# Optimization experiments

Hardware: AMD Instinct MI355X
Metric: run time of the kernel (lower is better)

## Reference

```python
import jax, jax.numpy as jnp
import numpy as np

B, N, C, H = 128, 8732, 512, 19  # batch, priors, channels, feature map side
IMG = 300.0
FG = 19


def setup_inputs() -> dict:
    key = jax.random.key(0)
    ks = jax.random.split(key, 10)
    loc = jax.random.normal(ks[0], (B, N, 4), jnp.float32) * 0.5
    conf = jax.random.normal(ks[1], (B, N, 2), jnp.float32)
    priors = jax.random.uniform(ks[2], (N, 4), jnp.float32, minval=0.05, maxval=0.95)
    features = jax.random.normal(ks[3], (B, C, H, H), jnp.float32)
    w1 = jax.random.normal(ks[4], (C, 4096), jnp.float32) * 0.01
    b1 = jnp.zeros((4096,), jnp.float32)
    w2 = jax.random.normal(ks[5], (4096, 4096), jnp.float32) * 0.01
    b2 = jnp.zeros((4096,), jnp.float32)
    w3 = jax.random.normal(ks[6], (4096, FG), jnp.float32) * 0.01
    b3 = jnp.zeros((FG,), jnp.float32)
    return {"loc": loc, "conf": conf, "priors": priors, "features": features,
            "w1": w1, "b1": b1, "w2": w2, "b2": b2, "w3": w3, "b3": b3}


def _decode(loc, priors):
    # SSD decode, variances=[0.1, 0.2]; priors are (cx, cy, w, h)
    cxcy = priors[:, :2] + loc[..., :2] * 0.1 * priors[:, 2:]
    wh = priors[:, 2:] * jnp.exp(loc[..., 2:] * 0.2)
    xy1 = cxcy - 0.5 * wh
    return jnp.concatenate([xy1, xy1 + wh], axis=-1)  # [B,N,4] corner form


def _best_prior(loc, conf, priors):
    boxes = _decode(loc, priors)                       # [B,N,4]
    probs = jax.nn.softmax(conf, axis=-1)              # [B,N,2]
    car = jnp.argmax(probs, axis=-1) == 1              # [B,N] argmax class == car
    score = jnp.where(car, probs[..., 1], -jnp.inf)
    best = jnp.argmax(score, axis=-1)                  # [B]
    best_box = jnp.take_along_axis(boxes, best[:, None, None], axis=1)[:, 0]  # [B,4]
    has_car = jnp.any(car, axis=-1)                    # [B]
    geom = (best_box[:, 2] > best_box[:, 0]) & (best_box[:, 3] > best_box[:, 1])
    valid = has_car & geom
    result = jnp.where(has_car[:, None], best_box, 0.0)
    result = jnp.clip(result, 0.0, 1.0)
    return result, valid


def _extract(features, boxes, valid):
    # per-box crop + global max pool -> [B,C], zero for invalid boxes
    ceil_num = features.shape[2]
    step = IMG / ceil_num
    b = jnp.clip(boxes * IMG, 0.0, IMG) / step
    b = jnp.floor(jnp.clip(b, 0.0, ceil_num - 1.0)).astype(jnp.int32)  # [B,4]=x1,y1,x2,y2
    r = jnp.arange(ceil_num)
    mh = (r[None, :] >= b[:, 1:2]) & (r[None, :] <= b[:, 3:4])  # [B,H] rows
    mw = (r[None, :] >= b[:, 0:1]) & (r[None, :] <= b[:, 2:3])  # [B,W] cols
    mask = mh[:, None, :, None] & mw[:, None, None, :]          # [B,1,H,W]
    m = jnp.max(jnp.where(mask, features, -jnp.inf), axis=(2, 3))  # [B,C]
    return jnp.where(valid[:, None], m, 0.0)


def reference(loc, conf, priors, features, w1, b1, w2, b2, w3, b3):
    boxes, valid = _best_prior(loc, conf, priors)
    feat = _extract(features, boxes, valid)             # [B,512]
    h = jax.nn.relu(feat @ w1 + b1)
    h = jax.nn.relu(h @ w2 + b2)
    fg_cls = h @ w3 + b3                                # [B,19]
    return fg_cls, boxes, valid.astype(jnp.int32)
```

## Files before the change

### kernel.cpp

```cpp
#include <hip/hip_runtime.h>
#include <hip/hip_bf16.h>
#include <math.h>

#define BATCH 128
#define NPRI  8732
#define CCH   512
#define HH    19
#define NHID  4096
#define FGC   19

typedef unsigned short ushort_t;
typedef __attribute__((ext_vector_type(8))) short bf16x8;
typedef __attribute__((ext_vector_type(4))) float f32x4;

__device__ __forceinline__ ushort_t f2bf(float f) {
  unsigned u = __float_as_uint(f);
  u += 0x7fff + ((u >> 16) & 1);
  return (ushort_t)(u >> 16);
}


__global__ void k_best_partial(const float* __restrict__ conf,
                               float* __restrict__ cs, int* __restrict__ ci,
                               int* __restrict__ cc) {
  int blk = blockIdx.x;
  int b = blk >> 2, chunk = blk & 3;
  int n0 = chunk * 2183;
  int t = threadIdx.x;
  const float* cb = conf + (size_t)b * NPRI * 2;
  float bestS = -INFINITY; int bestN = 0x7fffffff; int car_any = 0;
  for (int i = n0 + t; i < n0 + 2183; i += 256) {
    float c0 = cb[2 * i], c1 = cb[2 * i + 1];
    float m = fmaxf(c0, c1);
    float e0 = expf(c0 - m), e1 = expf(c1 - m);
    float s = e0 + e1;
    float p0 = e0 / s, p1 = e1 / s;
    bool car = p1 > p0;
    car_any |= (int)car;
    float sc = car ? p1 : -INFINITY;
    if (sc > bestS || (sc == bestS && i < bestN)) { bestS = sc; bestN = i; }
  }
  __shared__ float ls[256]; __shared__ int li[256]; __shared__ int lc[256];
  ls[t] = bestS; li[t] = bestN; lc[t] = car_any;
  __syncthreads();
  for (int off = 128; off > 0; off >>= 1) {
    if (t < off) {
      float s2 = ls[t + off]; int n2 = li[t + off];
      if (s2 > ls[t] || (s2 == ls[t] && n2 < li[t])) { ls[t] = s2; li[t] = n2; }
      lc[t] |= lc[t + off];
    }
    __syncthreads();
  }
  if (t == 0) { cs[blk] = ls[0]; ci[blk] = li[0]; cc[blk] = lc[0]; }
}

__global__ void k_best_final(const float* __restrict__ loc,
                             const float* __restrict__ priors,
                             const float* __restrict__ cs,
                             const int* __restrict__ ci,
                             const int* __restrict__ cc,
                             float* __restrict__ out_boxes,
                             float* __restrict__ out_valid,
                             int4* __restrict__ crop,
                             int* __restrict__ vflag) {
  int b = threadIdx.x;
  if (b >= BATCH) return;
  float bs = -INFINITY; int bn = 0; int hc = 0;
  #pragma unroll
  for (int p = 0; p < 4; p++) {
    float s = cs[b * 4 + p]; int n = ci[b * 4 + p];
    hc |= cc[b * 4 + p];
    if (s > bs) { bs = s; bn = n; }
  }
  const float* lp = loc + ((size_t)b * NPRI + bn) * 4;
  const float* pp = priors + (size_t)bn * 4;
  float l0 = lp[0], l1 = lp[1], l2 = lp[2], l3 = lp[3];
  float pcx = pp[0], pcy = pp[1], pw = pp[2], ph = pp[3];
  float cx = pcx + (l0 * 0.1f) * pw;
  float cy = pcy + (l1 * 0.1f) * ph;
  float w = pw * expf(l2 * 0.2f);
  float h = ph * expf(l3 * 0.2f);
  float x1 = cx - 0.5f * w;
  float y1 = cy - 0.5f * h;
  float x2 = x1 + w, y2 = y1 + h;
  bool geom = (x2 > x1) && (y2 > y1);
  bool valid = hc && geom;
  float r0, r1, r2, r3;
  if (hc) { r0 = x1; r1 = y1; r2 = x2; r3 = y2; }
  else    { r0 = r1 = r2 = r3 = 0.0f; }
  r0 = fminf(fmaxf(r0, 0.0f), 1.0f);
  r1 = fminf(fmaxf(r1, 0.0f), 1.0f);
  r2 = fminf(fmaxf(r2, 0.0f), 1.0f);
  r3 = fminf(fmaxf(r3, 0.0f), 1.0f);
  out_boxes[b * 4 + 0] = r0; out_boxes[b * 4 + 1] = r1;
  out_boxes[b * 4 + 2] = r2; out_boxes[b * 4 + 3] = r3;
  out_valid[b] = valid ? 1.0f : 0.0f;
  const float stepF = (float)(300.0 / 19.0);
  float q0 = fminf(fmaxf(r0 * 300.0f, 0.0f), 300.0f) / stepF;
  float q1 = fminf(fmaxf(r1 * 300.0f, 0.0f), 300.0f) / stepF;
  float q2 = fminf(fmaxf(r2 * 300.0f, 0.0f), 300.0f) / stepF;
  float q3 = fminf(fmaxf(r3 * 300.0f, 0.0f), 300.0f) / stepF;
  int ix1 = (int)floorf(fminf(fmaxf(q0, 0.0f), 18.0f));
  int iy1 = (int)floorf(fminf(fmaxf(q1, 0.0f), 18.0f));
  int ix2 = (int)floorf(fminf(fmaxf(q2, 0.0f), 18.0f));
  int iy2 = (int)floorf(fminf(fmaxf(q3, 0.0f), 18.0f));
  crop[b] = make_int4(ix1, iy1, ix2, iy2);
  vflag[b] = valid ? 1 : 0;
}

__global__ void k_extract(const float* __restrict__ fin,
                          const int4* __restrict__ crop,
                          const int* __restrict__ vflag,
                          ushort_t* __restrict__ feat) {
  int blk = blockIdx.x;
  int b = blk >> 7;
  int tile = blk & 127;
  int wave = threadIdx.x >> 6;
  int lane = threadIdx.x & 63;
  int c = tile * 4 + wave;
  if (!vflag[b]) {
    if (lane == 0) feat[b * CCH + c] = 0;
    return;
  }
  int4 cr = crop[b];
  int wcnt = cr.z - cr.x + 1;
  int cnt = wcnt * (cr.w - cr.y + 1);
  const float* p = fin + (size_t)(b * CCH + c) * (HH * HH);
  float m = -INFINITY;
  for (int i = lane; i < cnt; i += 64) {
    int yy = cr.y + i / wcnt;
    int xx = cr.x + i % wcnt;
    m = fmaxf(m, p[yy * HH + xx]);
  }
  #pragma unroll
  for (int off = 32; off > 0; off >>= 1) m = fmaxf(m, __shfl_xor(m, off));
  if (lane == 0) feat[b * CCH + c] = f2bf(m);
}

template <int KSPL>
__global__ __launch_bounds__(256) void k_mfma(const ushort_t* __restrict__ A,
                                              const float* __restrict__ W,
                                              float* __restrict__ part, int K) {
  const int N = 4096;
  const int BK = 32;
  int nb = blockIdx.x;
  int ks = blockIdx.y;
  int Kper = K / KSPL;
  int k0b = ks * Kper;
  int t = threadIdx.x;
  int lane = t & 63, wave = t >> 6;
  int q = lane >> 4, r = lane & 15;

  __shared__ ushort_t As[128 * 40];
  __shared__ ushort_t Bs[64 * 40];

  int wm = (wave & 1) * 64;
  int wn = (wave >> 1) * 32;
  int n0 = nb * 64;

  f32x4 acc[4][2];
  #pragma unroll
  for (int i = 0; i < 4; i++)
    #pragma unroll
    for (int j = 0; j < 2; j++) {
      acc[i][j].x = 0.f; acc[i][j].y = 0.f; acc[i][j].z = 0.f; acc[i][j].w = 0.f;
    }

  int am = t >> 1, ah = t & 1;
  int bp = t >> 4;
  int bn = t & 15;

  for (int k0 = k0b; k0 < k0b + Kper; k0 += BK) {
    const uint4* asrc = (const uint4*)(A + (size_t)am * K + k0 + ah * 16);
    uint4 a0 = asrc[0];
    uint4 a1 = asrc[1];
    const float* wsrc = W + (size_t)(k0 + 2 * bp) * N + n0 + bn;
    float wr0[4], wr1[4];
    #pragma unroll
    for (int i = 0; i < 4; i++) {
      wr0[i] = wsrc[16 * i];
      wr1[i] = wsrc[N + 16 * i];
    }
    __syncthreads();
    *(uint4*)&As[am * 40 + ah * 16]     = a0;
    *(uint4*)&As[am * 40 + ah * 16 + 8] = a1;
    #pragma unroll
    for (int i = 0; i < 4; i++) {
      unsigned pk = (unsigned)f2bf(wr0[i]) | ((unsigned)f2bf(wr1[i]) << 16);
      *(unsigned*)&Bs[(bn + 16 * i) * 40 + 2 * bp] = pk;
    }
    __syncthreads();
    bf16x8 af[4], bfr[2];
    #pragma unroll
    for (int i = 0; i < 4; i++)
      af[i] = *(const bf16x8*)&As[(wm + 16 * i + r) * 40 + q * 8];
    #pragma unroll
    for (int j = 0; j < 2; j++)
      bfr[j] = *(const bf16x8*)&Bs[(wn + 16 * j + r) * 40 + q * 8];
    #pragma unroll
    for (int i = 0; i < 4; i++)
      #pragma unroll
      for (int j = 0; j < 2; j++)
        acc[i][j] = __builtin_amdgcn_mfma_f32_16x16x32_bf16(af[i], bfr[j],
                                                            acc[i][j], 0, 0, 0);
  }

  float* dst = part + (size_t)ks * (BATCH * N);
  #pragma unroll
  for (int i = 0; i < 4; i++) {
    #pragma unroll
    for (int j = 0; j < 2; j++) {
      int col = n0 + wn + 16 * j + r;
      #pragma unroll
      for (int reg = 0; reg < 4; reg++) {
        int row = wm + 16 * i + q * 4 + reg;
        dst[(size_t)row * N + col] = acc[i][j][reg];
      }
    }
  }
}

template <int KSPL, bool BF16OUT>
__global__ void k_finalize(const float* __restrict__ part,
                           const float* __restrict__ bias,
                           float* __restrict__ outf,
                           ushort_t* __restrict__ outb) {
  int idx = (blockIdx.x * 256 + threadIdx.x) * 4;
  float4 s = *(const float4*)(part + idx);
  #pragma unroll
  for (int p = 1; p < KSPL; p++) {
    float4 v = *(const float4*)(part + (size_t)p * (BATCH * NHID) + idx);
    s.x += v.x; s.y += v.y; s.z += v.z; s.w += v.w;
  }
  float4 bv = *(const float4*)(bias + (idx & (NHID - 1)));
  s.x = fmaxf(s.x + bv.x, 0.0f); s.y = fmaxf(s.y + bv.y, 0.0f);
  s.z = fmaxf(s.z + bv.z, 0.0f); s.w = fmaxf(s.w + bv.w, 0.0f);
  if (BF16OUT) {
    ushort4 o;
    o.x = f2bf(s.x); o.y = f2bf(s.y); o.z = f2bf(s.z); o.w = f2bf(s.w);
    *(ushort4*)(outb + idx) = o;
  } else {
    *(float4*)(outf + idx) = s;
  }
}

__global__ void k_gemm3p(const float* __restrict__ h2,
                         const float* __restrict__ w3,
                         float* __restrict__ part3) {
  int kc = blockIdx.x;
  int t = threadIdx.x;
  __shared__ float wl[32 * FGC];
  for (int i = t; i < 32 * FGC; i += 128) wl[i] = w3[kc * 32 * FGC + i];
  __syncthreads();
  const float* hp = h2 + (size_t)t * NHID + kc * 32;
  float acc[FGC];
  #pragma unroll
  for (int j = 0; j < FGC; j++) acc[j] = 0.0f;
  for (int k = 0; k < 32; k++) {
    float hv = hp[k];
    const float* wp = &wl[k * FGC];
    #pragma unroll
    for (int j = 0; j < FGC; j++) acc[j] += hv * wp[j];
  }
  float* dst = part3 + (size_t)kc * (BATCH * FGC) + t * FGC;
  #pragma unroll
  for (int j = 0; j < FGC; j++) dst[j] = acc[j];
}

__global__ void k_fin3(const float* __restrict__ part3,
                       const float* __restrict__ b3,
                       float* __restrict__ out) {
  int j = blockIdx.x * 256 + threadIdx.x;
  if (j >= BATCH * FGC) return;
  float s = 0.0f;
  for (int p = 0; p < 128; p++) s += part3[(size_t)p * (BATCH * FGC) + j];
  out[j] = s + b3[j % FGC];
}

extern "C" void kernel_launch(void* const* d_in, const int* in_sizes, int n_in,
                              void* d_out, int out_size, void* d_ws, size_t ws_size,
                              hipStream_t stream) {
  const float* loc      = (const float*)d_in[0];
  const float* conf     = (const float*)d_in[1];
  const float* priors   = (const float*)d_in[2];
  const float* features = (const float*)d_in[3];
  const float* w1 = (const float*)d_in[4];
  const float* b1 = (const float*)d_in[5];
  const float* w2 = (const float*)d_in[6];
  const float* b2 = (const float*)d_in[7];
  const float* w3 = (const float*)d_in[8];
  const float* b3 = (const float*)d_in[9];
  float* out = (float*)d_out;

  char* ws = (char*)d_ws;
  float*    part  = (float*)ws;
  float*    part3 = (float*)(ws + (size_t)16 * 1024 * 1024);
  float*    h2    = (float*)(ws + (size_t)18 * 1024 * 1024);
  ushort_t* featb = (ushort_t*)(ws + (size_t)20 * 1024 * 1024);
  ushort_t* h1b   = (ushort_t*)(ws + (size_t)20 * 1024 * 1024 + 256 * 1024);
  float*    cs    = (float*)(ws + (size_t)21 * 1024 * 1024 + 512 * 1024);
  int*      ci    = (int*)(cs + 512);
  int*      cc    = ci + 512;
  int4*     crop  = (int4*)(cc + 512);
  int*      vfl   = (int*)(crop + BATCH);

  k_best_partial<<<512, 256, 0, stream>>>(conf, cs, ci, cc);
  k_best_final<<<1, 128, 0, stream>>>(loc, priors, cs, ci, cc,
                                      out + BATCH * FGC,
                                      out + BATCH * FGC + BATCH * 4, crop, vfl);
  k_extract<<<BATCH * (CCH / 4), 256, 0, stream>>>(features, crop, vfl, featb);
  k_mfma<4><<<dim3(64, 4), 256, 0, stream>>>(featb, w1, part, 512);
  k_finalize<4, true><<<512, 256, 0, stream>>>(part, b1, nullptr, h1b);
  k_mfma<8><<<dim3(64, 8), 256, 0, stream>>>(h1b, w2, part, 4096);
  k_finalize<8, false><<<512, 256, 0, stream>>>(part, b2, h2, nullptr);
  k_gemm3p<<<128, 128, 0, stream>>>(h2, w3, part3);
  k_fin3<<<10, 256, 0, stream>>>(part3, b3, out);
}
```

Baseline: 263.1 us.

## Merge best-prior kernels, vectorize extract, double-buffer MFMA GEMM, atomic final layer

```diff
diff --git a/kernel.cpp b/kernel.cpp
--- a/kernel.cpp
+++ b/kernel.cpp
@@ -1,5 +1,4 @@
 #include <hip/hip_runtime.h>
-#include <hip/hip_bf16.h>
 #include <math.h>
 
 #define BATCH 128
@@ -9,30 +8,31 @@
 #define NHID  4096
 #define FGC   19
 
-typedef unsigned short ushort_t;
+typedef unsigned short u16;
 typedef __attribute__((ext_vector_type(8))) short bf16x8;
 typedef __attribute__((ext_vector_type(4))) float f32x4;
 
-__device__ __forceinline__ ushort_t f2bf(float f) {
+__device__ __forceinline__ u16 f2bf(float f) {
   unsigned u = __float_as_uint(f);
   u += 0x7fff + ((u >> 16) & 1);
-  return (ushort_t)(u >> 16);
-}
-
-
-__global__ void k_best_partial(const float* __restrict__ conf,
-                               float* __restrict__ cs, int* __restrict__ ci,
-                               int* __restrict__ cc) {
-  int blk = blockIdx.x;
-  int b = blk >> 2, chunk = blk & 3;
-  int n0 = chunk * 2183;
+  return (u16)(u >> 16);
+}
+
+__global__ void k_best(const float* __restrict__ loc,
+                       const float* __restrict__ conf,
+                       const float* __restrict__ priors,
+                       const float* __restrict__ b3,
+                       float* __restrict__ out,
+                       int4* __restrict__ crop,
+                       int* __restrict__ vflag) {
+  int b = blockIdx.x;
   int t = threadIdx.x;
   const float* cb = conf + (size_t)b * NPRI * 2;
   float bestS = -INFINITY; int bestN = 0x7fffffff; int car_any = 0;
-  for (int i = n0 + t; i < n0 + 2183; i += 256) {
-    float c0 = cb[2 * i], c1 = cb[2 * i + 1];
-    float m = fmaxf(c0, c1);
-    float e0 = expf(c0 - m), e1 = expf(c1 - m);
+  for (int i = t; i < NPRI; i += 256) {
+    float2 c = *(const float2*)(cb + 2 * i);
+    float m = fmaxf(c.x, c.y);
+    float e0 = expf(c.x - m), e1 = expf(c.y - m);
     float s = e0 + e1;
     float p0 = e0 / s, p1 = e1 / s;
     bool car = p1 > p0;
@@ -51,112 +51,121 @@
     }
     __syncthreads();
   }
-  if (t == 0) { cs[blk] = ls[0]; ci[blk] = li[0]; cc[blk] = lc[0]; }
-}
-
-__global__ void k_best_final(const float* __restrict__ loc,
-                             const float* __restrict__ priors,
-                             const float* __restrict__ cs,
-                             const int* __restrict__ ci,
-                             const int* __restrict__ cc,
-                             float* __restrict__ out_boxes,
-                             float* __restrict__ out_valid,
-                             int4* __restrict__ crop,
-                             int* __restrict__ vflag) {
-  int b = threadIdx.x;
-  if (b >= BATCH) return;
-  float bs = -INFINITY; int bn = 0; int hc = 0;
-  #pragma unroll
-  for (int p = 0; p < 4; p++) {
-    float s = cs[b * 4 + p]; int n = ci[b * 4 + p];
-    hc |= cc[b * 4 + p];
-    if (s > bs) { bs = s; bn = n; }
-  }
-  const float* lp = loc + ((size_t)b * NPRI + bn) * 4;
-  const float* pp = priors + (size_t)bn * 4;
-  float l0 = lp[0], l1 = lp[1], l2 = lp[2], l3 = lp[3];
-  float pcx = pp[0], pcy = pp[1], pw = pp[2], ph = pp[3];
-  float cx = pcx + (l0 * 0.1f) * pw;
-  float cy = pcy + (l1 * 0.1f) * ph;
-  float w = pw * expf(l2 * 0.2f);
-  float h = ph * expf(l3 * 0.2f);
-  float x1 = cx - 0.5f * w;
-  float y1 = cy - 0.5f * h;
-  float x2 = x1 + w, y2 = y1 + h;
-  bool geom = (x2 > x1) && (y2 > y1);
-  bool valid = hc && geom;
-  float r0, r1, r2, r3;
-  if (hc) { r0 = x1; r1 = y1; r2 = x2; r3 = y2; }
-  else    { r0 = r1 = r2 = r3 = 0.0f; }
-  r0 = fminf(fmaxf(r0, 0.0f), 1.0f);
-  r1 = fminf(fmaxf(r1, 0.0f), 1.0f);
-  r2 = fminf(fmaxf(r2, 0.0f), 1.0f);
-  r3 = fminf(fmaxf(r3, 0.0f), 1.0f);
-  out_boxes[b * 4 + 0] = r0; out_boxes[b * 4 + 1] = r1;
-  out_boxes[b * 4 + 2] = r2; out_boxes[b * 4 + 3] = r3;
-  out_valid[b] = valid ? 1.0f : 0.0f;
-  const float stepF = (float)(300.0 / 19.0);
-  float q0 = fminf(fmaxf(r0 * 300.0f, 0.0f), 300.0f) / stepF;
-  float q1 = fminf(fmaxf(r1 * 300.0f, 0.0f), 300.0f) / stepF;
-  float q2 = fminf(fmaxf(r2 * 300.0f, 0.0f), 300.0f) / stepF;
-  float q3 = fminf(fmaxf(r3 * 300.0f, 0.0f), 300.0f) / stepF;
-  int ix1 = (int)floorf(fminf(fmaxf(q0, 0.0f), 18.0f));
-  int iy1 = (int)floorf(fminf(fmaxf(q1, 0.0f), 18.0f));
-  int ix2 = (int)floorf(fminf(fmaxf(q2, 0.0f), 18.0f));
-  int iy2 = (int)floorf(fminf(fmaxf(q3, 0.0f), 18.0f));
-  crop[b] = make_int4(ix1, iy1, ix2, iy2);
-  vflag[b] = valid ? 1 : 0;
+  if (t < FGC) out[b * FGC + t] = b3[t];
+  if (t == 0) {
+    int hc = lc[0];
+    int bn = hc ? li[0] : 0;
+    const float* lp = loc + ((size_t)b * NPRI + bn) * 4;
+    const float* pp = priors + (size_t)bn * 4;
+    float l0 = lp[0], l1 = lp[1], l2 = lp[2], l3 = lp[3];
+    float pcx = pp[0], pcy = pp[1], pw = pp[2], ph = pp[3];
+    float cx = pcx + (l0 * 0.1f) * pw;
+    float cy = pcy + (l1 * 0.1f) * ph;
+    float w = pw * expf(l2 * 0.2f);
+    float h = ph * expf(l3 * 0.2f);
+    float x1 = cx - 0.5f * w;
+    float y1 = cy - 0.5f * h;
+    float x2 = x1 + w, y2 = y1 + h;
+    bool geom = (x2 > x1) && (y2 > y1);
+    bool valid = hc && geom;
+    float r0, r1, r2, r3;
+    if (hc) { r0 = x1; r1 = y1; r2 = x2; r3 = y2; }
+    else    { r0 = r1 = r2 = r3 = 0.0f; }
+    r0 = fminf(fmaxf(r0, 0.0f), 1.0f);
+    r1 = fminf(fmaxf(r1, 0.0f), 1.0f);
+    r2 = fminf(fmaxf(r2, 0.0f), 1.0f);
+    r3 = fminf(fmaxf(r3, 0.0f), 1.0f);
+    float* ob = out + BATCH * FGC;
+    ob[b * 4 + 0] = r0; ob[b * 4 + 1] = r1;
+    ob[b * 4 + 2] = r2; ob[b * 4 + 3] = r3;
+    out[BATCH * FGC + BATCH * 4 + b] = valid ? 1.0f : 0.0f;
+    const float stepF = (float)(300.0 / 19.0);
+    float q0 = fminf(fmaxf(r0 * 300.0f, 0.0f), 300.0f) / stepF;
+    float q1 = fminf(fmaxf(r1 * 300.0f, 0.0f), 300.0f) / stepF;
+    float q2 = fminf(fmaxf(r2 * 300.0f, 0.0f), 300.0f) / stepF;
+    float q3 = fminf(fmaxf(r3 * 300.0f, 0.0f), 300.0f) / stepF;
+    int ix1 = (int)floorf(fminf(fmaxf(q0, 0.0f), 18.0f));
+    int iy1 = (int)floorf(fminf(fmaxf(q1, 0.0f), 18.0f));
+    int ix2 = (int)floorf(fminf(fmaxf(q2, 0.0f), 18.0f));
+    int iy2 = (int)floorf(fminf(fmaxf(q3, 0.0f), 18.0f));
+    crop[b] = make_int4(ix1, iy1, ix2, iy2);
+    vflag[b] = valid ? 1 : 0;
+  }
 }
 
 __global__ void k_extract(const float* __restrict__ fin,
                           const int4* __restrict__ crop,
                           const int* __restrict__ vflag,
-                          ushort_t* __restrict__ feat) {
-  int blk = blockIdx.x;
-  int b = blk >> 7;
-  int tile = blk & 127;
-  int wave = threadIdx.x >> 6;
-  int lane = threadIdx.x & 63;
-  int c = tile * 4 + wave;
+                          u16* __restrict__ feat) {
+  int b = blockIdx.x >> 3;
+  int cg = blockIdx.x & 7;
+  int wave = threadIdx.x >> 6, lane = threadIdx.x & 63;
   if (!vflag[b]) {
-    if (lane == 0) feat[b * CCH + c] = 0;
+    if (lane == 0) {
+      #pragma unroll
+      for (int ci = 0; ci < 16; ci++) feat[b * CCH + cg * 64 + ci * 4 + wave] = 0;
+    }
     return;
   }
   int4 cr = crop[b];
-  int wcnt = cr.z - cr.x + 1;
-  int cnt = wcnt * (cr.w - cr.y + 1);
-  const float* p = fin + (size_t)(b * CCH + c) * (HH * HH);
-  float m = -INFINITY;
-  for (int i = lane; i < cnt; i += 64) {
-    int yy = cr.y + i / wcnt;
-    int xx = cr.x + i % wcnt;
-    m = fmaxf(m, p[yy * HH + xx]);
-  }
-  #pragma unroll
-  for (int off = 32; off > 0; off >>= 1) m = fmaxf(m, __shfl_xor(m, off));
-  if (lane == 0) feat[b * CCH + c] = f2bf(m);
+  int base = cr.y * HH;
+  int L = (cr.w - cr.y + 1) * HH;
+  int a0 = base & ~3;
+  int offs = base - a0;
+  int total = offs + L;
+  int nf4 = total >> 2, rem = total & 3;
+  int x1 = cr.x, x2 = cr.z;
+  #pragma unroll 4
+  for (int ci = 0; ci < 16; ci++) {
+    int c = cg * 64 + ci * 4 + wave;
+    const float* p = fin + (size_t)(b * CCH + c) * (HH * HH) + a0;
+    float m = -INFINITY;
+    for (int i = lane; i < nf4; i += 64) {
+      float4 v = *(const float4*)(p + 4 * i);
+      int e = a0 + 4 * i;
+      #pragma unroll
+      for (int j = 0; j < 4; j++) {
+        int ej = e + j;
+        int x = ej % HH;
+        bool in = (ej >= base) && (x >= x1) && (x <= x2);
+        float f = j == 0 ? v.x : (j == 1 ? v.y : (j == 2 ? v.z : v.w));
+        m = in ? fmaxf(m, f) : m;
+      }
+    }
+    if (lane < rem) {
+      int ej = a0 + 4 * nf4 + lane;
+      int x = ej % HH;
+      if (ej >= base && x >= x1 && x <= x2) m = fmaxf(m, p[4 * nf4 + lane]);
+    }
+    #pragma unroll
+    for (int off = 32; off > 0; off >>= 1) m = fmaxf(m, __shfl_xor(m, off));
+    if (lane == 0) feat[b * CCH + c] = f2bf(m);
+  }
 }
 
 template <int KSPL>
-__global__ __launch_bounds__(256) void k_mfma(const ushort_t* __restrict__ A,
-                                              const float* __restrict__ W,
-                                              float* __restrict__ part, int K) {
-  const int N = 4096;
-  const int BK = 32;
-  int nb = blockIdx.x;
-  int ks = blockIdx.y;
-  int Kper = K / KSPL;
-  int k0b = ks * Kper;
-  int t = threadIdx.x;
-  int lane = t & 63, wave = t >> 6;
+__global__ __launch_bounds__(256, 2) void k_mfma(const u16* __restrict__ A,
+                                                 const float* __restrict__ W,
+                                                 float* __restrict__ part, int K) {
+  const int N = NHID, BK = 32, ST = 40;
+  __shared__ u16 As[2][128 * ST];
+  __shared__ u16 Bs[2][64 * ST];
+  int nb = blockIdx.x, ks = blockIdx.y;
+  int Kper = K / KSPL, k0b = ks * Kper;
+  int t = threadIdx.x, lane = t & 63, wave = t >> 6;
   int q = lane >> 4, r = lane & 15;
-
-  __shared__ ushort_t As[128 * 40];
-  __shared__ ushort_t Bs[64 * 40];
-
-  int wm = (wave & 1) * 64;
-  int wn = (wave >> 1) * 32;
-  int n0 = nb * 64;
+  int wm = (wave & 1) * 64, wn = (wave >> 1) * 32, n0 = nb * 64;
+
+  int am = t >> 1, ah = (t & 1) * 16;
+  int kp = t >> 4, n4 = (t & 15) * 4;
+
+  const u16* aptr = A + (size_t)am * K + k0b + ah;
+  const float* wptr = W + (size_t)(k0b + 2 * kp) * N + n0 + n4;
+
+  uint4 a0 = *(const uint4*)aptr;
+  uint4 a1 = *(const uint4*)(aptr + 8);
+  float4 w0 = *(const float4*)wptr;
+  float4 w1 = *(const float4*)(wptr + N);
 
   f32x4 acc[4][2];
   #pragma unroll
@@ -166,48 +175,63 @@
       acc[i][j].x = 0.f; acc[i][j].y = 0.f; acc[i][j].z = 0.f; acc[i][j].w = 0.f;
     }
 
-  int am = t >> 1, ah = t & 1;
-  int bp = t >> 4;
-  int bn = t & 15;
-
-  for (int k0 = k0b; k0 < k0b + Kper; k0 += BK) {
-    const uint4* asrc = (const uint4*)(A + (size_t)am * K + k0 + ah * 16);
-    uint4 a0 = asrc[0];
-    uint4 a1 = asrc[1];
-    const float* wsrc = W + (size_t)(k0 + 2 * bp) * N + n0 + bn;
-    float wr0[4], wr1[4];
-    #pragma unroll
-    for (int i = 0; i < 4; i++) {
-      wr0[i] = wsrc[16 * i];
-      wr1[i] = wsrc[N + 16 * i];
-    }
+  *(uint4*)&As[0][am * ST + ah]     = a0;
+  *(uint4*)&As[0][am * ST + ah + 8] = a1;
+  {
+    unsigned pk0 = (unsigned)f2bf(w0.x) | ((unsigned)f2bf(w1.x) << 16);
+    unsigned pk1 = (unsigned)f2bf(w0.y) | ((unsigned)f2bf(w1.y) << 16);
+    unsigned pk2 = (unsigned)f2bf(w0.z) | ((unsigned)f2bf(w1.z) << 16);
+    unsigned pk3 = (unsigned)f2bf(w0.w) | ((unsigned)f2bf(w1.w) << 16);
+    *(unsigned*)&Bs[0][(n4 + 0) * ST + 2 * kp] = pk0;
+    *(unsigned*)&Bs[0][(n4 + 1) * ST + 2 * kp] = pk1;
+    *(unsigned*)&Bs[0][(n4 + 2) * ST + 2 * kp] = pk2;
+    *(unsigned*)&Bs[0][(n4 + 3) * ST + 2 * kp] = pk3;
+  }
+
+  int nIter = Kper / BK;
+  for (int it = 0; it < nIter; it++) {
     __syncthreads();
-    *(uint4*)&As[am * 40 + ah * 16]     = a0;
-    *(uint4*)&As[am * 40 + ah * 16 + 8] = a1;
-    #pragma unroll
-    for (int i = 0; i < 4; i++) {
-      unsigned pk = (unsigned)f2bf(wr0[i]) | ((unsigned)f2bf(wr1[i]) << 16);
-      *(unsigned*)&Bs[(bn + 16 * i) * 40 + 2 * bp] = pk;
-    }
-    __syncthreads();
+    int cur = it & 1;
+    bool more = (it + 1 < nIter);
+    if (more) {
+      aptr += BK;
+      wptr += (size_t)BK * N;
+      a0 = *(const uint4*)aptr;
+      a1 = *(const uint4*)(aptr + 8);
+      w0 = *(const float4*)wptr;
+      w1 = *(const float4*)(wptr + N);
+    }
     bf16x8 af[4], bfr[2];
     #pragma unroll
     for (int i = 0; i < 4; i++)
-      af[i] = *(const bf16x8*)&As[(wm + 16 * i + r) * 40 + q * 8];
+      af[i] = *(const bf16x8*)&As[cur][(wm + 16 * i + r) * ST + q * 8];
     #pragma unroll
     for (int j = 0; j < 2; j++)
-      bfr[j] = *(const bf16x8*)&Bs[(wn + 16 * j + r) * 40 + q * 8];
+      bfr[j] = *(const bf16x8*)&Bs[cur][(wn + 16 * j + r) * ST + q * 8];
     #pragma unroll
     for (int i = 0; i < 4; i++)
       #pragma unroll
       for (int j = 0; j < 2; j++)
         acc[i][j] = __builtin_amdgcn_mfma_f32_16x16x32_bf16(af[i], bfr[j],
                                                             acc[i][j], 0, 0, 0);
+    if (more) {
+      int nxt = cur ^ 1;
+      *(uint4*)&As[nxt][am * ST + ah]     = a0;
+      *(uint4*)&As[nxt][am * ST + ah + 8] = a1;
+      unsigned pk0 = (unsigned)f2bf(w0.x) | ((unsigned)f2bf(w1.x) << 16);
+      unsigned pk1 = (unsigned)f2bf(w0.y) | ((unsigned)f2bf(w1.y) << 16);
+      unsigned pk2 = (unsigned)f2bf(w0.z) | ((unsigned)f2bf(w1.z) << 16);
+      unsigned pk3 = (unsigned)f2bf(w0.w) | ((unsigned)f2bf(w1.w) << 16);
+      *(unsigned*)&Bs[nxt][(n4 + 0) * ST + 2 * kp] = pk0;
+      *(unsigned*)&Bs[nxt][(n4 + 1) * ST + 2 * kp] = pk1;
+      *(unsigned*)&Bs[nxt][(n4 + 2) * ST + 2 * kp] = pk2;
+      *(unsigned*)&Bs[nxt][(n4 + 3) * ST + 2 * kp] = pk3;
+    }
   }
 
   float* dst = part + (size_t)ks * (BATCH * N);
   #pragma unroll
-  for (int i = 0; i < 4; i++) {
+  for (int i = 0; i < 4; i++)
     #pragma unroll
     for (int j = 0; j < 2; j++) {
       int col = n0 + wn + 16 * j + r;
@@ -217,14 +241,13 @@
         dst[(size_t)row * N + col] = acc[i][j][reg];
       }
     }
-  }
 }
 
 template <int KSPL, bool BF16OUT>
 __global__ void k_finalize(const float* __restrict__ part,
                            const float* __restrict__ bias,
                            float* __restrict__ outf,
-                           ushort_t* __restrict__ outb) {
+                           u16* __restrict__ outb) {
   int idx = (blockIdx.x * 256 + threadIdx.x) * 4;
   float4 s = *(const float4*)(part + idx);
   #pragma unroll
@@ -244,37 +267,27 @@
   }
 }
 
-__global__ void k_gemm3p(const float* __restrict__ h2,
+__global__ void k_gemm3a(const float* __restrict__ h2,
                          const float* __restrict__ w3,
-                         float* __restrict__ part3) {
+                         float* __restrict__ out) {
   int kc = blockIdx.x;
   int t = threadIdx.x;
-  __shared__ float wl[32 * FGC];
-  for (int i = t; i < 32 * FGC; i += 128) wl[i] = w3[kc * 32 * FGC + i];
+  __shared__ float wl[128 * FGC];
+  for (int i = t; i < 128 * FGC; i += 256) wl[i] = w3[kc * 128 * FGC + i];
   __syncthreads();
-  const float* hp = h2 + (size_t)t * NHID + kc * 32;
+  int m = t & 127, half = t >> 7;
+  const float* hp = h2 + (size_t)m * NHID + kc * 128 + half * 64;
   float acc[FGC];
   #pragma unroll
   for (int j = 0; j < FGC; j++) acc[j] = 0.0f;
-  for (int k = 0; k < 32; k++) {
+  for (int k = 0; k < 64; k++) {
     float hv = hp[k];
-    const float* wp = &wl[k * FGC];
+    const float* wp = &wl[(half * 64 + k) * FGC];
     #pragma unroll
     for (int j = 0; j < FGC; j++) acc[j] += hv * wp[j];
   }
-  float* dst = part3 + (size_t)kc * (BATCH * FGC) + t * FGC;
-  #pragma unroll
-  for (int j = 0; j < FGC; j++) dst[j] = acc[j];
-}
-
-__global__ void k_fin3(const float* __restrict__ part3,
-                       const float* __restrict__ b3,
-                       float* __restrict__ out) {
-  int j = blockIdx.x * 256 + threadIdx.x;
-  if (j >= BATCH * FGC) return;
-  float s = 0.0f;
-  for (int p = 0; p < 128; p++) s += part3[(size_t)p * (BATCH * FGC) + j];
-  out[j] = s + b3[j % FGC];
+  #pragma unroll
+  for (int j = 0; j < FGC; j++) atomicAdd(&out[m * FGC + j], acc[j]);
 }
 
 extern "C" void kernel_launch(void* const* d_in, const int* in_sizes, int n_in,
@@ -293,26 +306,18 @@
   float* out = (float*)d_out;
 
   char* ws = (char*)d_ws;
-  float*    part  = (float*)ws;
-  float*    part3 = (float*)(ws + (size_t)16 * 1024 * 1024);
-  float*    h2    = (float*)(ws + (size_t)18 * 1024 * 1024);
-  ushort_t* featb = (ushort_t*)(ws + (size_t)20 * 1024 * 1024);
-  ushort_t* h1b   = (ushort_t*)(ws + (size_t)20 * 1024 * 1024 + 256 * 1024);
-  float*    cs    = (float*)(ws + (size_t)21 * 1024 * 1024 + 512 * 1024);
-  int*      ci    = (int*)(cs + 512);
-  int*      cc    = ci + 512;
-  int4*     crop  = (int4*)(cc + 512);
-  int*      vfl   = (int*)(crop + BATCH);
-
-  k_best_partial<<<512, 256, 0, stream>>>(conf, cs, ci, cc);
-  k_best_final<<<1, 128, 0, stream>>>(loc, priors, cs, ci, cc,
-                                      out + BATCH * FGC,
-                                      out + BATCH * FGC + BATCH * 4, crop, vfl);
-  k_extract<<<BATCH * (CCH / 4), 256, 0, stream>>>(features, crop, vfl, featb);
+  float* part  = (float*)ws;
+  float* h2    = (float*)(ws + (size_t)16 * 1024 * 1024);
+  u16*   featb = (u16*)(ws + (size_t)18 * 1024 * 1024);
+  u16*   h1b   = (u16*)(ws + (size_t)18 * 1024 * 1024 + 512 * 1024);
+  int4*  crop  = (int4*)(ws + (size_t)20 * 1024 * 1024);
+  int*   vfl   = (int*)(crop + BATCH);
+
+  k_best<<<BATCH, 256, 0, stream>>>(loc, conf, priors, b3, out, crop, vfl);
+  k_extract<<<BATCH * 8, 256, 0, stream>>>(features, crop, vfl, featb);
   k_mfma<4><<<dim3(64, 4), 256, 0, stream>>>(featb, w1, part, 512);
   k_finalize<4, true><<<512, 256, 0, stream>>>(part, b1, nullptr, h1b);
   k_mfma<8><<<dim3(64, 8), 256, 0, stream>>>(h1b, w2, part, 4096);
   k_finalize<8, false><<<512, 256, 0, stream>>>(part, b2, h2, nullptr);
-  k_gemm3p<<<128, 128, 0, stream>>>(h2, w3, part3);
-  k_fin3<<<10, 256, 0, stream>>>(part3, b3, out);
-}
+  k_gemm3a<<<32, 256, 0, stream>>>(h2, w3, out);
+}
```

After: 305.3 us. +16.0%, slower.
